# Kernel tuning notes

Measured on AMD Instinct MI355X. Metric: run time of the kernel, lower is better.

Reference implementation:

```python
import jax, jax.numpy as jnp
import numpy as np

N_HEADS = 16


def setup_inputs() -> dict:
    key = jax.random.key(0)
    ks = jax.random.split(key, 5)
    B, S, D = 4, 1024, 1024
    H = N_HEADS
    hs = D // H
    sc = 0.02
    return {
        "x": jax.random.normal(ks[0], (B, S, D), jnp.float32),
        "Wqkv": jax.random.normal(ks[1], (3 * D, D), jnp.float32) * sc,
        "Wout": jax.random.normal(ks[2], (D, D), jnp.float32) * sc,
        "Wpos": jax.random.normal(ks[3], (D, D), jnp.float32) * sc,
        "posn_vect_u": jnp.zeros((1, H, 1, hs), jnp.float32),
        "posn_vect_v": jnp.zeros((1, H, 1, hs), jnp.float32),
        "rel_embed": jax.random.normal(ks[4], (S, D), jnp.float32) * sc,
    }


def reference(x, Wqkv, Wout, Wpos, posn_vect_u, posn_vect_v, rel_embed):
    B, S, D = x.shape
    H = N_HEADS
    hs = D // H

    # qkv projection (torch Linear: y = x @ W.T), split into q,k,v
    qkv = x @ Wqkv.T  # [B,S,3D]
    q, k, v = jnp.split(qkv, 3, axis=-1)
    # [B,S,D] -> [B,H,S,hs]
    q = q.reshape(B, S, H, hs).transpose(0, 2, 1, 3)
    k = k.reshape(B, S, H, hs).transpose(0, 2, 1, 3)
    v = v.reshape(B, S, H, hs).transpose(0, 2, 1, 3)

    # content term: (q + u) @ k^T -> [B,H,S,S]
    attn_dots = jnp.einsum("bhqd,bhkd->bhqk", q + posn_vect_u, k)

    # relative position term (Transformer-XL style)
    rel = rel_embed[-S:] @ Wpos.T          # [S,D]
    rel = rel.T.reshape(H, hs, S)          # [H,hs,S]
    query_posn = jnp.einsum("bhqd,hdk->bhqk", q + posn_vect_v, rel)  # [B,H,S,S]

    # rel-shift gather: shifted[i,j] = query_posn[i, j - i + S - 1]
    i = jnp.arange(S)[:, None]
    j = jnp.arange(S)[None, :]
    idx = jnp.clip(j - i + S - 1, 0, S - 1)  # [S,S]; entries with j>i masked later
    shifted = jnp.take_along_axis(query_posn, idx[None, None], axis=-1)
    attn_dots = attn_dots + shifted

    # causal mask then scaled softmax (matches masked_fill then softmax(x/sqrt(hs)))
    causal = j > i  # [S,S] True above diagonal
    attn_dots = jnp.where(causal[None, None], -jnp.inf, attn_dots)
    scores = jax.nn.softmax(attn_dots / np.sqrt(hs).astype(np.float32), axis=-1)

    attn = jnp.einsum("bhqk,bhkd->bhqd", scores, v)  # [B,H,S,hs]
    out = attn.transpose(0, 2, 1, 3).reshape(B, S, D) @ Wout.T
    return out
```

## Files before the change

### kernel.cpp

```cpp
#include <hip/hip_runtime.h>

#define S_LEN 1024

typedef unsigned short u16;
using bf16x8 = __attribute__((ext_vector_type(8))) short;
using f32x4  = __attribute__((ext_vector_type(4))) float;
using u16x8  = __attribute__((ext_vector_type(8))) unsigned short;
using u16x4  = __attribute__((ext_vector_type(4))) unsigned short;
using u32x4  = __attribute__((ext_vector_type(4))) unsigned int;

__device__ __forceinline__ float bf2f(u16 b) {
  unsigned int u = ((unsigned int)b) << 16;
  return __builtin_bit_cast(float, u);
}
__device__ __forceinline__ u16 f2bf(float f) {
  unsigned int u = __builtin_bit_cast(unsigned int, f);
  unsigned int r = u + 0x7fffu + ((u >> 16) & 1u);
  return (u16)(r >> 16);
}
__device__ __forceinline__ unsigned int cvtpk(float lo, float hi) {
  unsigned int r;
  asm("v_cvt_pk_bf16_f32 %0, %1, %2" : "=v"(r) : "v"(lo), "v"(hi));
  return r;
}
__device__ __forceinline__ float fmax3(float a, float b, float c) {
  return fmaxf(fmaxf(a, b), c);
}

using gas_p = const __attribute__((address_space(1))) void*;
using las_p = __attribute__((address_space(3))) void*;
__device__ __forceinline__ void gload16(const void* g, void* l) {
  __builtin_amdgcn_global_load_lds((gas_p)g, (las_p)l, 16, 0, 0);
}

__global__ __launch_bounds__(256) void cvt_all(const float* __restrict__ x,
    const float* __restrict__ wqkv, const float* __restrict__ wout,
    const float* __restrict__ wpos, const float* __restrict__ rel,
    u16* __restrict__ xb, u16* __restrict__ wqkvb, u16* __restrict__ woutb,
    u16* __restrict__ wposb, u16* __restrict__ relb) {
  int blk = blockIdx.x;
  const float* src; u16* dst; int base;
  if (blk < 4096)      { src = x;    dst = xb;    base = blk; }
  else if (blk < 7168) { src = wqkv; dst = wqkvb; base = blk - 4096; }
  else if (blk < 8192) { src = wout; dst = woutb; base = blk - 7168; }
  else if (blk < 9216) { src = wpos; dst = wposb; base = blk - 8192; }
  else                 { src = rel;  dst = relb;  base = blk - 9216; }
  int i = (base * 256 + threadIdx.x) * 4;
  float4 v = *(const float4*)(src + i);
  u16x4 o;
  o.x = f2bf(v.x); o.y = f2bf(v.y); o.z = f2bf(v.z); o.w = f2bf(v.w);
  *(u16x4*)(dst + i) = o;
}

template <int MODE, int SWZ, int BM64>
__global__ __launch_bounds__(256) void gemm_bt(const u16* __restrict__ A,
    const u16* __restrict__ W, float* __restrict__ Yf, u16* __restrict__ Yb,
    u16* __restrict__ qc, u16* __restrict__ qp,
    const float* __restrict__ uvec, const float* __restrict__ vvec,
    int M, int N, int K) {
  constexpr int BM = BM64 ? 64 : 128;
  constexpr int MI = BM64 ? 2 : 4;
  __shared__ __align__(16) u16 As[2][BM * 32];
  __shared__ __align__(16) u16 Ws[2][128 * 32];
  const int t = threadIdx.x;
  const int w = t >> 6, l = t & 63;
  const int lr = l & 15, lg = l >> 4;
  int bm, bn;
  if (SWZ == 1) {
    int flat = (int)blockIdx.y * 32 + (int)blockIdx.x;
    int xcd = flat & 7, idx = flat >> 3;
    bm = (xcd & 3) * 8 + (idx & 7);
    bn = (xcd >> 2) * 12 + (idx >> 3);
  } else {
    bm = blockIdx.x; bn = blockIdx.y;
  }
  const int wr = BM64 ? ((w >> 1) * 32) : ((w >> 1) * 64);
  const int wc = (w & 1) * 64;
  f32x4 acc[MI][4];
#pragma unroll
  for (int mi = 0; mi < MI; ++mi)
#pragma unroll
    for (int ni = 0; ni < 4; ++ni) acc[mi][ni] = (f32x4){0.f, 0.f, 0.f, 0.f};
  const u16* Ab = A + (size_t)bm * BM * K;
  const u16* Wb = W + (size_t)bn * 128 * K;

  auto stage = [&](int k0, int buf) {
#pragma unroll
    for (int i = 0; i < (BM64 ? 1 : 2); ++i) {
      int c = i * 256 + t;
      gload16(Ab + (size_t)(c >> 2) * K + k0 + (c & 3) * 8, &As[buf][c * 8]);
    }
#pragma unroll
    for (int i = 0; i < 2; ++i) {
      int c = i * 256 + t;
      gload16(Wb + (size_t)(c >> 2) * K + k0 + (c & 3) * 8, &Ws[buf][c * 8]);
    }
  };

  stage(0, 0);
  __syncthreads();
  for (int k0 = 0; k0 < K; k0 += 32) {
    const int cur = (k0 >> 5) & 1;
    if (k0 + 32 < K) stage(k0 + 32, cur ^ 1);
    bf16x8 af[MI], wf[4];
#pragma unroll
    for (int mi = 0; mi < MI; ++mi)
      af[mi] = *(const bf16x8*)&As[cur][(wr + mi * 16 + lr) * 32 + lg * 8];
#pragma unroll
    for (int ni = 0; ni < 4; ++ni)
      wf[ni] = *(const bf16x8*)&Ws[cur][(wc + ni * 16 + lr) * 32 + lg * 8];
    __builtin_amdgcn_s_setprio(1);
#pragma unroll
    for (int mi = 0; mi < MI; ++mi)
#pragma unroll
      for (int ni = 0; ni < 4; ++ni)
        acc[mi][ni] = __builtin_amdgcn_mfma_f32_16x16x32_bf16(af[mi], wf[ni], acc[mi][ni], 0, 0, 0);
    __builtin_amdgcn_s_setprio(0);
    __syncthreads();
  }
#pragma unroll
  for (int mi = 0; mi < MI; ++mi)
#pragma unroll
    for (int ni = 0; ni < 4; ++ni) {
      int col = bn * 128 + wc + ni * 16 + lr;
      if (MODE == 1) {
#pragma unroll
        for (int g = 0; g < 4; ++g) {
          int row = bm * BM + wr + mi * 16 + lg * 4 + g;
          Yf[(size_t)row * N + col] = acc[mi][ni][g];
        }
      } else if (MODE == 0) {
#pragma unroll
        for (int g = 0; g < 4; ++g) {
          int row = bm * BM + wr + mi * 16 + lg * 4 + g;
          Yb[(size_t)row * N + col] = f2bf(acc[mi][ni][g]);
        }
      } else {
        if (col < 1024) {
          float uu = uvec[col], vv = vvec[col];
#pragma unroll
          for (int g = 0; g < 4; ++g) {
            int row = bm * BM + wr + mi * 16 + lg * 4 + g;
            qc[(size_t)row * 1024 + col] = f2bf((acc[mi][ni][g] + uu) * 0.125f);
            qp[(size_t)row * 1024 + col] = f2bf((acc[mi][ni][g] + vv) * 0.125f);
          }
        } else if (col < 2048) {
#pragma unroll
          for (int g = 0; g < 4; ++g) {
            int row = bm * BM + wr + mi * 16 + lg * 4 + g;
            Yb[(size_t)row * 3072 + col] = f2bf(acc[mi][ni][g]);
          }
        } else {
          int row0 = bm * BM + wr + mi * 16 + lg * 4;
          int vrow = (row0 >> 10) * 1024 + (col - 2048);
          u16x4 tmp;
#pragma unroll
          for (int g = 0; g < 4; ++g) tmp[g] = f2bf(acc[mi][ni][g]);
          *(u16x4*)&Yb[(size_t)vrow * 3072 + (row0 & 1023)] = tmp;
        }
      }
    }
}

__global__ __launch_bounds__(256) void attn_fwd(
    const u16* __restrict__ qcb, const u16* __restrict__ qpb,
    const u16* __restrict__ qkv, const u16* __restrict__ relp,
    u16* __restrict__ out) {
  __shared__ __align__(16) u16 Ksb[2][4096];
  __shared__ __align__(16) u16 Vtb[2][4096];
  __shared__ __align__(16) u16 Rs3[3][4096];
  __shared__ __align__(16) float Psf[4][16][68];

  const int flat = (int)blockIdx.y * 8 + (int)blockIdx.x;
  const int wg = (flat & 7) * 64 + (flat >> 3);
  const int sub = wg & 7;
  const int bh = wg >> 3;
  const int b = bh >> 4, h = bh & 15;
  const int t = threadIdx.x;
  const int w = t >> 6, l = t & 63;
  const int lr = l & 15, lg = l >> 4;

  const u16* Kg = qkv + (size_t)b * S_LEN * 3072 + 1024 + h * 64;
  const u16* Vg = qkv + (size_t)bh * 64 * 3072;
  const u16* Rg = relp + h * 64;

  int gl4[4], cg[4];
#pragma unroll
  for (int g = 0; g < 4; ++g) {
    int ql = lg * 4 + g;
    gl4[g] = (l & 48) | ((lr - ql - 1) & 15);
    cg[g] = (lr > ql) ? 1 : 0;
  }

  for (int half = 0; half < 2; ++half) {
    const int qt = half ? sub : (15 - sub);
    const int i0 = qt * 64;
    const int nt = qt + 1;

    bf16x8 qcf[2], qpf[2];
    {
      size_t qoff = (size_t)(b * S_LEN + i0 + w * 16 + lr) * 1024 + h * 64;
      qcf[0] = *(const bf16x8*)(qcb + qoff + lg * 8);
      qcf[1] = *(const bf16x8*)(qcb + qoff + 32 + lg * 8);
      qpf[0] = *(const bf16x8*)(qpb + qoff + lg * 8);
      qpf[1] = *(const bf16x8*)(qpb + qoff + 32 + lg * 8);
    }

    auto stage_k = [&](int j0s, int buf) {
#pragma unroll
      for (int i = 0; i < 2; ++i) {
        int bK = i * 4 + w;
        int ttk = bK >> 1, kc = bK & 1;
        gload16(Kg + (size_t)(j0s + ttk * 16 + lr) * 3072 + kc * 32 + lg * 8,
                &Ksb[buf][bK * 512 + l * 8]);
      }
    };
    auto stage_v = [&](int j0s, int buf) {
#pragma unroll
      for (int i = 0; i < 2; ++i) {
        int bV = i * 4 + w;
        int dt = bV >> 1, kc = bV & 1;
        gload16(Vg + (size_t)(dt * 16 + lr) * 3072 + j0s + kc * 32 + lg * 8,
                &Vtb[buf][bV * 512 + l * 8]);
      }
    };
    auto stage_rchunk = [&](int Gloc, int slot) {
      int Gg = 15 - qt + Gloc;
#pragma unroll
      for (int i = 0; i < 2; ++i) {
        int bR = i * 4 + w;
        int btc = bR >> 1, kc = bR & 1;
        int r = Gg * 64 + btc * 16 + lr;
        r = r > S_LEN - 1 ? S_LEN - 1 : r;
        gload16(Rg + (size_t)r * 1024 + kc * 32 + lg * 8,
                &Rs3[slot][bR * 512 + l * 8]);
      }
    };

    float m_run = -1e30f, l_run = 0.f;
    f32x4 o_acc[4];
#pragma unroll
    for (int dt = 0; dt < 4; ++dt) o_acc[dt] = (f32x4){0.f, 0.f, 0.f, 0.f};

    stage_k(0, 0);
    stage_v(0, 0);
    stage_rchunk(0, 0);
    stage_rchunk(1, 1);
    __syncthreads();

    int sA = 0, sB = 1, sC = 2;
    for (int kt = 0; kt < nt; ++kt) {
      const int cur = kt & 1, nxt = cur ^ 1;
      const int j0 = kt * 64;
      const int have_nxt = (kt + 1 < nt);
      if (have_nxt) {
        stage_k(j0 + 64, nxt);
        stage_v(j0 + 64, nxt);
        stage_rchunk(kt + 2, sC);
      }

      f32x4 sc[4];
      __builtin_amdgcn_s_setprio(1);
#pragma unroll
      for (int tt = 0; tt < 4; ++tt) {
        sc[tt] = (f32x4){0.f, 0.f, 0.f, 0.f};
#pragma unroll
        for (int kc = 0; kc < 2; ++kc) {
          bf16x8 kf = *(const bf16x8*)&Ksb[cur][(tt * 2 + kc) * 512 + l * 8];
          sc[tt] = __builtin_amdgcn_mfma_f32_16x16x32_bf16(qcf[kc], kf, sc[tt], 0, 0, 0);
        }
      }
      f32x4 sp[5];
#pragma unroll
      for (int u5 = 0; u5 < 5; ++u5) {
        int bt = 3 - w + u5;
        const u16* rb = (bt & 4) ? &Rs3[sB][0] : &Rs3[sA][0];
        int btc = bt & 3;
        sp[u5] = (f32x4){0.f, 0.f, 0.f, 0.f};
#pragma unroll
        for (int kc = 0; kc < 2; ++kc) {
          bf16x8 rf = *(const bf16x8*)&rb[(btc * 2 + kc) * 512 + l * 8];
          sp[u5] = __builtin_amdgcn_mfma_f32_16x16x32_bf16(qpf[kc], rf, sp[u5], 0, 0, 0);
        }
      }
      __builtin_amdgcn_s_setprio(0);

#pragma unroll
      for (int g = 0; g < 4; ++g) {
        float bp[5];
#pragma unroll
        for (int u5 = 0; u5 < 5; ++u5) bp[u5] = __shfl(sp[u5][g], gl4[g]);
#pragma unroll
        for (int tt = 0; tt < 4; ++tt)
          sc[tt][g] += cg[g] ? bp[tt + 1] : bp[tt];
      }
      if (kt == nt - 1) {
#pragma unroll
        for (int g = 0; g < 4; ++g) {
          int iw = i0 + w * 16 + lg * 4 + g;
#pragma unroll
          for (int tt = 0; tt < 4; ++tt)
            if (j0 + tt * 16 + lr > iw) sc[tt][g] = -1e30f;
        }
      }
#pragma unroll
      for (int g = 0; g < 4; ++g)
#pragma unroll
        for (int tt = 0; tt < 4; ++tt)
          Psf[w][lg * 4 + g][tt * 16 + lr] = sc[tt][g];

      float zz[2][8];
#pragma unroll
      for (int kc = 0; kc < 2; ++kc)
#pragma unroll
        for (int h4 = 0; h4 < 2; ++h4) {
          float4 rv = *(const float4*)&Psf[w][lr][kc * 32 + lg * 8 + h4 * 4];
          zz[kc][h4 * 4 + 0] = rv.x; zz[kc][h4 * 4 + 1] = rv.y;
          zz[kc][h4 * 4 + 2] = rv.z; zz[kc][h4 * 4 + 3] = rv.w;
        }
      float ma = fmax3(zz[0][0], zz[0][1], zz[0][2]);
      float mb = fmax3(zz[0][3], zz[0][4], zz[0][5]);
      float mc = fmax3(zz[0][6], zz[0][7], zz[1][0]);
      float md = fmax3(zz[1][1], zz[1][2], zz[1][3]);
      float me = fmax3(zz[1][4], zz[1][5], zz[1][6]);
      float mt = fmax3(ma, mb, zz[1][7]);
      mt = fmax3(mt, mc, md);
      mt = fmaxf(mt, me);
      mt = fmaxf(mt, __shfl_xor(mt, 16));
      mt = fmaxf(mt, __shfl_xor(mt, 32));
      float mnew = fmaxf(m_run, mt);
      float corr = __expf(m_run - mnew);
      m_run = mnew;
#pragma unroll
      for (int kc = 0; kc < 2; ++kc)
#pragma unroll
        for (int j = 0; j < 8; ++j) zz[kc][j] = __expf(zz[kc][j] - mnew);
      float s;
      {
        float a0 = zz[0][0] + zz[0][1], a1 = zz[0][2] + zz[0][3];
        float a2 = zz[0][4] + zz[0][5], a3 = zz[0][6] + zz[0][7];
        float a4 = zz[1][0] + zz[1][1], a5 = zz[1][2] + zz[1][3];
        float a6 = zz[1][4] + zz[1][5], a7 = zz[1][6] + zz[1][7];
        float b0 = a0 + a1, b1 = a2 + a3, b2 = a4 + a5, b3 = a6 + a7;
        s = (b0 + b1) + (b2 + b3);
      }
      s += __shfl_xor(s, 16);
      s += __shfl_xor(s, 32);
      l_run = l_run * corr + s;

      float co[4];
#pragma unroll
      for (int g = 0; g < 4; ++g) co[g] = __shfl(corr, lg * 4 + g);
#pragma unroll
      for (int dt = 0; dt < 4; ++dt)
#pragma unroll
        for (int g = 0; g < 4; ++g) o_acc[dt][g] *= co[g];

      bf16x8 pf[2];
#pragma unroll
      for (int kc = 0; kc < 2; ++kc) {
        u32x4 pw;
#pragma unroll
        for (int j2 = 0; j2 < 4; ++j2)
          pw[j2] = cvtpk(zz[kc][j2 * 2], zz[kc][j2 * 2 + 1]);
        pf[kc] = __builtin_bit_cast(bf16x8, pw);
      }

      __builtin_amdgcn_s_setprio(1);
#pragma unroll
      for (int dt = 0; dt < 4; ++dt) {
#pragma unroll
        for (int kc = 0; kc < 2; ++kc) {
          bf16x8 vf = *(const bf16x8*)&Vtb[cur][(dt * 2 + kc) * 512 + l * 8];
          o_acc[dt] = __builtin_amdgcn_mfma_f32_16x16x32_bf16(pf[kc], vf, o_acc[dt], 0, 0, 0);
        }
      }
      __builtin_amdgcn_s_setprio(0);
      __syncthreads();
      int stmp = sA; sA = sB; sB = sC; sC = stmp;
    }

    float ll[4];
#pragma unroll
    for (int g = 0; g < 4; ++g) ll[g] = __shfl(l_run, lg * 4 + g);
#pragma unroll
    for (int dt = 0; dt < 4; ++dt) {
      int col = h * 64 + dt * 16 + lr;
#pragma unroll
      for (int g = 0; g < 4; ++g) {
        int row = b * S_LEN + i0 + w * 16 + lg * 4 + g;
        out[(size_t)row * 1024 + col] = f2bf(o_acc[dt][g] / ll[g]);
      }
    }
  }
}

extern "C" void kernel_launch(void* const* d_in, const int* in_sizes, int n_in,
                              void* d_out, int out_size, void* d_ws, size_t ws_size,
                              hipStream_t stream) {
  const float* x    = (const float*)d_in[0];
  const float* Wqkv = (const float*)d_in[1];
  const float* Wout = (const float*)d_in[2];
  const float* Wpos = (const float*)d_in[3];
  const float* u    = (const float*)d_in[4];
  const float* v    = (const float*)d_in[5];
  const float* rel  = (const float*)d_in[6];
  float* out = (float*)d_out;

  u16* ws      = (u16*)d_ws;
  u16* xb      = ws;
  u16* wqkvb   = xb + 4194304;
  u16* woutb   = wqkvb + 3145728;
  u16* wposb   = woutb + 1048576;
  u16* relb    = wposb + 1048576;
  u16* qkvb    = relb + 1048576;
  u16* qcb     = qkvb + 12582912;
  u16* qpb     = qcb + 4194304;
  u16* relproj = qpb + 4194304;
  u16* attno   = relproj + 1048576;

  cvt_all<<<10240, 256, 0, stream>>>(x, Wqkv, Wout, Wpos, rel, xb, wqkvb, woutb, wposb, relb);

  gemm_bt<2, 1, 0><<<dim3(32, 24), 256, 0, stream>>>(xb, wqkvb, nullptr, qkvb, qcb, qpb, u, v, 4096, 3072, 1024);
  gemm_bt<0, 0, 1><<<dim3(16, 8), 256, 0, stream>>>(relb, wposb, nullptr, relproj, nullptr, nullptr, nullptr, nullptr, 1024, 1024, 1024);
  attn_fwd<<<dim3(8, 64), 256, 0, stream>>>(qcb, qpb, qkvb, relproj, attno);
  gemm_bt<1, 0, 1><<<dim3(64, 8), 256, 0, stream>>>(attno, woutb, out, nullptr, nullptr, nullptr, nullptr, nullptr, 4096, 1024, 1024);
}
```

Measured before the change: 137.5 us.

## Use lazy softmax rescaling and LDS atomics for the rel-shift add

Replaces the per-tile online-softmax max/rescale with a lazy scheme. Exponentials are taken against the running max, the PV MFMA is issued right away, and the accumulator and denominator are rescaled only when the tile maximum exceeds a threshold (about e^8). The shuffle-based rel-shift gather of positional scores is replaced by LDS atomicAdds into the score scratch tile, and the causal mask moves to after the LDS reload. This removes the max reduction and correction multiplies from the critical path before the PV MFMA. In exchange it relies on bounded score magnitudes for numerical safety and adds LDS atomic traffic.

```diff
diff --git a/kernel.cpp b/kernel.cpp
--- a/kernel.cpp
+++ b/kernel.cpp
@@ -184,14 +184,6 @@
   const u16* Vg = qkv + (size_t)bh * 64 * 3072;
   const u16* Rg = relp + h * 64;
 
-  int gl4[4], cg[4];
-#pragma unroll
-  for (int g = 0; g < 4; ++g) {
-    int ql = lg * 4 + g;
-    gl4[g] = (l & 48) | ((lr - ql - 1) & 15);
-    cg[g] = (lr > ql) ? 1 : 0;
-  }
-
   for (int half = 0; half < 2; ++half) {
     const int qt = half ? sub : (15 - sub);
     const int i0 = qt * 64;
@@ -237,7 +229,7 @@
       }
     };
 
-    float m_run = -1e30f, l_run = 0.f;
+    float m_run = 0.f, l_run = 0.f;
     f32x4 o_acc[4];
 #pragma unroll
     for (int dt = 0; dt < 4; ++dt) o_acc[dt] = (f32x4){0.f, 0.f, 0.f, 0.f};
@@ -286,28 +278,19 @@
       __builtin_amdgcn_s_setprio(0);
 
 #pragma unroll
-      for (int g = 0; g < 4; ++g) {
-        float bp[5];
-#pragma unroll
-        for (int u5 = 0; u5 < 5; ++u5) bp[u5] = __shfl(sp[u5][g], gl4[g]);
-#pragma unroll
-        for (int tt = 0; tt < 4; ++tt)
-          sc[tt][g] += cg[g] ? bp[tt + 1] : bp[tt];
-      }
-      if (kt == nt - 1) {
-#pragma unroll
-        for (int g = 0; g < 4; ++g) {
-          int iw = i0 + w * 16 + lg * 4 + g;
-#pragma unroll
-          for (int tt = 0; tt < 4; ++tt)
-            if (j0 + tt * 16 + lr > iw) sc[tt][g] = -1e30f;
-        }
-      }
-#pragma unroll
       for (int g = 0; g < 4; ++g)
 #pragma unroll
         for (int tt = 0; tt < 4; ++tt)
           Psf[w][lg * 4 + g][tt * 16 + lr] = sc[tt][g];
+#pragma unroll
+      for (int u5 = 0; u5 < 5; ++u5)
+#pragma unroll
+        for (int g = 0; g < 4; ++g) {
+          int ql = lg * 4 + g;
+          int kl = u5 * 16 + lr + ql - 15;
+          if ((unsigned)kl < 64u)
+            atomicAdd(&Psf[w][ql][kl], sp[u5][g]);
+        }
 
       float zz[2][8];
 #pragma unroll
@@ -318,64 +301,76 @@
           zz[kc][h4 * 4 + 0] = rv.x; zz[kc][h4 * 4 + 1] = rv.y;
           zz[kc][h4 * 4 + 2] = rv.z; zz[kc][h4 * 4 + 3] = rv.w;
         }
-      float ma = fmax3(zz[0][0], zz[0][1], zz[0][2]);
-      float mb = fmax3(zz[0][3], zz[0][4], zz[0][5]);
-      float mc = fmax3(zz[0][6], zz[0][7], zz[1][0]);
-      float md = fmax3(zz[1][1], zz[1][2], zz[1][3]);
-      float me = fmax3(zz[1][4], zz[1][5], zz[1][6]);
-      float mt = fmax3(ma, mb, zz[1][7]);
-      mt = fmax3(mt, mc, md);
-      mt = fmaxf(mt, me);
-      mt = fmaxf(mt, __shfl_xor(mt, 16));
-      mt = fmaxf(mt, __shfl_xor(mt, 32));
-      float mnew = fmaxf(m_run, mt);
-      float corr = __expf(m_run - mnew);
-      m_run = mnew;
+      if (kt == nt - 1) {
+        int iglob = i0 + w * 16 + lr;
+#pragma unroll
+        for (int kc = 0; kc < 2; ++kc)
+#pragma unroll
+          for (int j = 0; j < 8; ++j)
+            if (j0 + kc * 32 + lg * 8 + j > iglob) zz[kc][j] = -1e30f;
+      }
+
 #pragma unroll
       for (int kc = 0; kc < 2; ++kc)
 #pragma unroll
-        for (int j = 0; j < 8; ++j) zz[kc][j] = __expf(zz[kc][j] - mnew);
-      float s;
+        for (int j = 0; j < 8; ++j) zz[kc][j] = __expf(zz[kc][j] - m_run);
+      bf16x8 pf[2];
+#pragma unroll
+      for (int kc = 0; kc < 2; ++kc) {
+        u32x4 pw;
+#pragma unroll
+        for (int j2 = 0; j2 < 4; ++j2)
+          pw[j2] = cvtpk(zz[kc][j2 * 2], zz[kc][j2 * 2 + 1]);
+        pf[kc] = __builtin_bit_cast(bf16x8, pw);
+      }
+      __builtin_amdgcn_s_setprio(1);
+#pragma unroll
+      for (int dt = 0; dt < 4; ++dt) {
+#pragma unroll
+        for (int kc = 0; kc < 2; ++kc) {
+          bf16x8 vf = *(const bf16x8*)&Vtb[cur][(dt * 2 + kc) * 512 + l * 8];
+          o_acc[dt] = __builtin_amdgcn_mfma_f32_16x16x32_bf16(pf[kc], vf, o_acc[dt], 0, 0, 0);
+        }
+      }
+      __builtin_amdgcn_s_setprio(0);
+
+      float s, em;
       {
         float a0 = zz[0][0] + zz[0][1], a1 = zz[0][2] + zz[0][3];
         float a2 = zz[0][4] + zz[0][5], a3 = zz[0][6] + zz[0][7];
         float a4 = zz[1][0] + zz[1][1], a5 = zz[1][2] + zz[1][3];
         float a6 = zz[1][4] + zz[1][5], a7 = zz[1][6] + zz[1][7];
-        float b0 = a0 + a1, b1 = a2 + a3, b2 = a4 + a5, b3 = a6 + a7;
-        s = (b0 + b1) + (b2 + b3);
+        s = ((a0 + a1) + (a2 + a3)) + ((a4 + a5) + (a6 + a7));
+        float m0 = fmax3(zz[0][0], zz[0][1], zz[0][2]);
+        float m1 = fmax3(zz[0][3], zz[0][4], zz[0][5]);
+        float m2 = fmax3(zz[0][6], zz[0][7], zz[1][0]);
+        float m3 = fmax3(zz[1][1], zz[1][2], zz[1][3]);
+        float m4 = fmax3(zz[1][4], zz[1][5], zz[1][6]);
+        em = fmax3(m0, m1, zz[1][7]);
+        em = fmax3(em, m2, m3);
+        em = fmaxf(em, m4);
       }
       s += __shfl_xor(s, 16);
       s += __shfl_xor(s, 32);
-      l_run = l_run * corr + s;
-
-      float co[4];
-#pragma unroll
-      for (int g = 0; g < 4; ++g) co[g] = __shfl(corr, lg * 4 + g);
-#pragma unroll
-      for (int dt = 0; dt < 4; ++dt)
-#pragma unroll
-        for (int g = 0; g < 4; ++g) o_acc[dt][g] *= co[g];
-
-      bf16x8 pf[2];
-#pragma unroll
-      for (int kc = 0; kc < 2; ++kc) {
-        u32x4 pw;
-#pragma unroll
-        for (int j2 = 0; j2 < 4; ++j2)
-          pw[j2] = cvtpk(zz[kc][j2 * 2], zz[kc][j2 * 2 + 1]);
-        pf[kc] = __builtin_bit_cast(bf16x8, pw);
-      }
-
-      __builtin_amdgcn_s_setprio(1);
-#pragma unroll
-      for (int dt = 0; dt < 4; ++dt) {
-#pragma unroll
-        for (int kc = 0; kc < 2; ++kc) {
-          bf16x8 vf = *(const bf16x8*)&Vtb[cur][(dt * 2 + kc) * 512 + l * 8];
-          o_acc[dt] = __builtin_amdgcn_mfma_f32_16x16x32_bf16(pf[kc], vf, o_acc[dt], 0, 0, 0);
-        }
-      }
-      __builtin_amdgcn_s_setprio(0);
+      em = fmaxf(em, __shfl_xor(em, 16));
+      em = fmaxf(em, __shfl_xor(em, 32));
+
+      if (__all(em <= 2980.958f)) {
+        l_run += s;
+      } else {
+        float lem = __logf(fmaxf(em, 1.f));
+        float corr = __expf(-lem);
+        m_run += lem;
+        l_run = (l_run + s) * corr;
+        float co[4];
+#pragma unroll
+        for (int g = 0; g < 4; ++g) co[g] = __shfl(corr, lg * 4 + g);
+#pragma unroll
+        for (int dt = 0; dt < 4; ++dt)
+#pragma unroll
+          for (int g = 0; g < 4; ++g) o_acc[dt][g] *= co[g];
+      }
+
       __syncthreads();
       int stmp = sA; sA = sB; sB = sC; sC = stmp;
     }
```

New measurement: 304.0 us. 2.21x slower.
